# Performance work log

Hardware: AMD Instinct MI355X
Metric: run time of the kernel (lower is better)

The kernel has to match this reference:

```python
import jax, jax.numpy as jnp
import numpy as np

B, T, E, F, K = 4, 1024, 768, 24576, 32


def setup_inputs() -> dict:
    key = jax.random.key(0)
    k1, k2, k3 = jax.random.split(key, 3)
    x = jax.random.normal(k1, (B, T, E), dtype=jnp.float32)
    # kaiming_uniform-ish init for W_dec; W_enc initialized as W_dec.T (as in the module)
    bound = float(np.sqrt(6.0 / F))
    W_dec = jax.random.uniform(k2, (F, E), dtype=jnp.float32, minval=-bound, maxval=bound)
    W_enc = W_dec.T
    b_enc = jnp.zeros((F,), dtype=jnp.float32)
    b_dec = jnp.zeros((E,), dtype=jnp.float32)
    return {"x": x, "W_enc": W_enc, "W_dec": W_dec, "b_enc": b_enc, "b_dec": b_dec, "k": K}


def reference(x, W_enc, W_dec, b_enc, b_dec, k):
    # encode: (B,T,E) @ (E,F) -> (B,T,F)
    latent = jnp.einsum("bte,ef->btf", x - b_dec, W_enc) + b_enc
    # top-k mask: keep values >= k-th largest along feature dim
    kth = jax.lax.top_k(latent, k)[0][..., -1:]  # (B,T,1)
    feature_magnitudes = latent * (latent >= kth).astype(latent.dtype)
    # decode: (B,T,F) @ (F,E) -> (B,T,E)
    x_reconstructed = jnp.einsum("btf,fe->bte", feature_magnitudes, W_dec) + b_dec
    return x_reconstructed, feature_magnitudes
```

## Files before the change

kernel.cpp:

```cpp
#include <hip/hip_runtime.h>
#include <stdint.h>

#define BT_TOK 4096
#define EDIM 768
#define FDIM 24576

__device__ __forceinline__ uint32_t f2u(float f) {
    uint32_t b = __float_as_uint(f);
    return (b & 0x80000000u) ? ~b : (b | 0x80000000u);
}
__device__ __forceinline__ float u2f(uint32_t u) {
    uint32_t b = (u & 0x80000000u) ? (u & 0x7FFFFFFFu) : ~u;
    return __uint_as_float(b);
}

#define GBM 128
#define GBN 128
#define NSEG (FDIM / GBN)
#define SEGW 32
#define SEGCAP 15
#define SEGPRE (NSEG * SEGW)
#define ZCB (SEGPRE / GBN)
#define BANDCAP 160
#define T0 0.6f
#define DELTA2 0.035f

typedef int   i32x4 __attribute__((ext_vector_type(4)));
typedef float f32x4 __attribute__((ext_vector_type(4)));

__global__ __launch_bounds__(256)
void build_A_i8(const float* __restrict__ x, const float* __restrict__ bdec,
                unsigned char* __restrict__ Ai8, float* __restrict__ sxr)
{
    const int w = threadIdx.x >> 6, lane = threadIdx.x & 63;
    const int row = blockIdx.x * 4 + w;
    const float* src = x + (size_t)row * EDIM + lane * 12;
    const float* bd  = bdec + lane * 12;
    float d[12];
    #pragma unroll
    for (int t = 0; t < 3; ++t) {
        float4 v = *(const float4*)(src + t * 4);
        float4 b = *(const float4*)(bd + t * 4);
        d[t*4+0] = v.x - b.x; d[t*4+1] = v.y - b.y;
        d[t*4+2] = v.z - b.z; d[t*4+3] = v.w - b.w;
    }
    float m = 0.f;
    #pragma unroll
    for (int j = 0; j < 12; ++j) m = fmaxf(m, fabsf(d[j]));
    #pragma unroll
    for (int s = 1; s < 64; s <<= 1) m = fmaxf(m, __shfl_xor(m, s, 64));
    const float inv = (m > 0.f) ? 127.f / m : 0.f;
    if (lane == 0) sxr[row] = m / 127.f;
    uint32_t* po = (uint32_t*)(Ai8 + (size_t)row * EDIM) + lane * 3;
    #pragma unroll
    for (int t = 0; t < 3; ++t) {
        uint32_t pk = 0;
        #pragma unroll
        for (int j = 0; j < 4; ++j) {
            int q = (int)rintf(d[t*4+j] * inv);
            q = (q > 127) ? 127 : ((q < -127) ? -127 : q);
            pk |= ((uint32_t)(q & 255)) << (8 * j);
        }
        po[t] = pk;
    }
}

#define TT 64
__global__ __launch_bounds__(256)
void build_WT(const float* __restrict__ Wenc, float* __restrict__ WTf)
{
    __shared__ float tile[TT][TT + 4];
    const int n0 = blockIdx.x * TT, k0 = blockIdx.y * TT;
    const int t = threadIdx.x;

    const int krow = t >> 2, cseg = (t & 3) * 16;
    const float* src = Wenc + (size_t)(k0 + krow) * FDIM + n0 + cseg;
    float4 a0 = *(const float4*)(src);
    float4 a1 = *(const float4*)(src + 4);
    float4 a2 = *(const float4*)(src + 8);
    float4 a3 = *(const float4*)(src + 12);
    *(float4*)&tile[krow][cseg]      = a0;
    *(float4*)&tile[krow][cseg + 4]  = a1;
    *(float4*)&tile[krow][cseg + 8]  = a2;
    *(float4*)&tile[krow][cseg + 12] = a3;
    __syncthreads();

    const int nrow = t >> 2, kseg = (t & 3) * 16;
    float vals[16];
    #pragma unroll
    for (int i = 0; i < 16; ++i) vals[i] = tile[kseg + i][nrow];
    const size_t orow = (size_t)(n0 + nrow) * EDIM + k0 + kseg;
    #pragma unroll
    for (int i = 0; i < 16; i += 4)
        *(float4*)(WTf + orow + i) = make_float4(vals[i], vals[i+1], vals[i+2], vals[i+3]);
}

__global__ __launch_bounds__(256)
void quantW_i8(const float* __restrict__ WTf, unsigned char* __restrict__ Wi8,
               float* __restrict__ sw)
{
    const int w = threadIdx.x >> 6, lane = threadIdx.x & 63;
    const int row = blockIdx.x * 4 + w;
    const float* src = WTf + (size_t)row * EDIM + lane * 12;
    float d[12];
    #pragma unroll
    for (int t = 0; t < 3; ++t) {
        float4 v = *(const float4*)(src + t * 4);
        d[t*4+0] = v.x; d[t*4+1] = v.y; d[t*4+2] = v.z; d[t*4+3] = v.w;
    }
    float m = 0.f;
    #pragma unroll
    for (int j = 0; j < 12; ++j) m = fmaxf(m, fabsf(d[j]));
    #pragma unroll
    for (int s = 1; s < 64; s <<= 1) m = fmaxf(m, __shfl_xor(m, s, 64));
    const float inv = (m > 0.f) ? 127.f / m : 0.f;
    if (lane == 0) sw[row] = m / 127.f;
    uint32_t* po = (uint32_t*)(Wi8 + (size_t)row * EDIM) + lane * 3;
    #pragma unroll
    for (int t = 0; t < 3; ++t) {
        uint32_t pk = 0;
        #pragma unroll
        for (int j = 0; j < 4; ++j) {
            int q = (int)rintf(d[t*4+j] * inv);
            q = (q > 127) ? 127 : ((q < -127) ? -127 : q);
            pk |= ((uint32_t)(q & 255)) << (8 * j);
        }
        po[t] = pk;
    }
}

__device__ __forceinline__ void gld16(const unsigned char* g, void* l) {
    __builtin_amdgcn_global_load_lds(
        (const __attribute__((address_space(1))) void*)g,
        (__attribute__((address_space(3))) void*)l, 16, 0, 0);
}

__global__ __launch_bounds__(256)
void encode_i8_cand(const unsigned char* __restrict__ A,
                    const unsigned char* __restrict__ BT,
                    const float* __restrict__ benc,
                    const float* __restrict__ sxr,
                    const float* __restrict__ sw,
                    float* __restrict__ fm)
{
    __shared__ int As_i[3 * 2048];
    __shared__ int Bs_i[3 * 2048];
    __shared__ int rowcnt[GBM];

    const int tid = threadIdx.x;
    const int l = tid & 63, w = tid >> 6;
    const int wrow = (w >> 1) * 64, wcol = (w & 1) * 64;
    const int lr = l & 15, lg = l >> 4;
    const int bm = blockIdx.y * GBM, bn = blockIdx.x * GBN;
    const int cb = blockIdx.x;

    const int r0 = tid & 127, g0 = tid >> 7;
    const unsigned char* gA0 = A  + (size_t)(bm + r0) * EDIM + g0 * 16;
    const unsigned char* gA1 = A  + (size_t)(bm + r0) * EDIM + (g0 + 2) * 16;
    const unsigned char* gB0 = BT + (size_t)(bn + r0) * EDIM + g0 * 16;
    const unsigned char* gB1 = BT + (size_t)(bn + r0) * EDIM + (g0 + 2) * 16;
    int* lA0 = As_i + tid * 4;
    int* lA1 = As_i + (tid + 256) * 4;
    int* lB0 = Bs_i + tid * 4;
    int* lB1 = Bs_i + (tid + 256) * 4;

    i32x4 acc[4][4];
    #pragma unroll
    for (int i = 0; i < 4; ++i)
        #pragma unroll
        for (int j = 0; j < 4; ++j)
            acc[i][j] = (i32x4){0, 0, 0, 0};

    for (int st = 0; st < 4; ++st) {
        __syncthreads();
        #pragma unroll
        for (int t = 0; t < 3; ++t) {
            const int kt = st * 3 + t;
            gld16(gA0 + kt * 64, lA0 + t * 2048);
            gld16(gA1 + kt * 64, lA1 + t * 2048);
            gld16(gB0 + kt * 64, lB0 + t * 2048);
            gld16(gB1 + kt * 64, lB1 + t * 2048);
        }
        __syncthreads();

        #pragma unroll
        for (int t = 0; t < 3; ++t) {
            i32x4 af[4], bfr[4];
            #pragma unroll
            for (int f = 0; f < 4; ++f) {
                af[f]  = *(const i32x4*)&As_i[t * 2048 + (lg * 128 + wrow + f * 16 + lr) * 4];
                bfr[f] = *(const i32x4*)&Bs_i[t * 2048 + (lg * 128 + wcol + f * 16 + lr) * 4];
            }
            #pragma unroll
            for (int fi = 0; fi < 4; ++fi)
                #pragma unroll
                for (int fj = 0; fj < 4; ++fj)
                    acc[fi][fj] = __builtin_amdgcn_mfma_i32_16x16x64_i8(
                        af[fi], bfr[fj], acc[fi][fj], 0, 0, 0);
        }
    }

    for (int i = tid; i < GBM; i += 256) rowcnt[i] = 0;
    __syncthreads();

    float bev[4], swv[4];
    #pragma unroll
    for (int fj = 0; fj < 4; ++fj) {
        const int c = bn + wcol + fj * 16 + lr;
        bev[fj] = benc[c];
        swv[fj] = sw[c];
    }

    #pragma unroll
    for (int fi = 0; fi < 4; ++fi) {
        #pragma unroll
        for (int q = 0; q < 4; ++q) {
            const int rl = wrow + fi * 16 + lg * 4 + q;
            const float srow = sxr[bm + rl];
            uint32_t* seg = (uint32_t*)(fm + (size_t)(bm + rl) * FDIM) + (size_t)cb * SEGW;
            #pragma unroll
            for (int fj = 0; fj < 4; ++fj) {
                const float v = (float)acc[fi][fj][q] * (srow * swv[fj]) + bev[fj];
                if (v > T0) {
                    const int c = bn + wcol + fj * 16 + lr;
                    int p = atomicAdd(&rowcnt[rl], 1);
                    if (p < SEGCAP) {
                        seg[1 + p] = f2u(v);
                        seg[1 + SEGCAP + p] = (uint32_t)c;
                    }
                }
            }
        }
    }
    __syncthreads();
    for (int i = tid; i < GBM; i += 256) {
        uint32_t* seg = (uint32_t*)(fm + (size_t)(bm + i) * FDIM) + (size_t)cb * SEGW;
        seg[0] = (uint32_t)rowcnt[i];
    }

    if (cb >= ZCB) {
        const float4 z4 = make_float4(0.f, 0.f, 0.f, 0.f);
        const int rz = tid >> 5, cz = (tid & 31) * 4;
        #pragma unroll
        for (int p = 0; p < 16; ++p)
            *(float4*)(fm + (size_t)(bm + p * 8 + rz) * FDIM + bn + cz) = z4;
    }
}

__device__ __forceinline__ void sort512(uint32_t* ckey, uint32_t* cidx, int tid) {
    for (int ksz = 2; ksz <= 512; ksz <<= 1) {
        for (int j = ksz >> 1; j > 0; j >>= 1) {
            for (int i = tid; i < 512; i += 256) {
                const int ixj = i ^ j;
                if (ixj > i) {
                    uint32_t ka = ckey[i], kb = ckey[ixj];
                    uint32_t ia = cidx[i], ib = cidx[ixj];
                    bool after = (ka < kb) || (ka == kb && ia > ib);
                    bool descBlock = ((i & ksz) == 0);
                    if (descBlock ? after : !after) {
                        ckey[i] = kb; ckey[ixj] = ka;
                        cidx[i] = ib; cidx[ixj] = ia;
                    }
                }
            }
            __syncthreads();
        }
    }
}

__global__ __launch_bounds__(256)
void topk2(float* __restrict__ fm, float* __restrict__ xrec,
           const float* __restrict__ x, const float* __restrict__ WTf,
           const float* __restrict__ Wenc, const float* __restrict__ Wdec,
           const float* __restrict__ benc, const float* __restrict__ bdec,
           const int* __restrict__ kptr)
{
    const int row = blockIdx.x;
    const int tid = threadIdx.x;
    float* lrow = fm + (size_t)row * FDIM;
    const uint32_t* lrowu = (const uint32_t*)lrow;
    const float* xr = x + (size_t)row * EDIM;
    int kk = *kptr;
    if (kk < 1) kk = 1;
    if (kk > 511) kk = 511;

    __shared__ uint32_t ckey[512];
    __shared__ uint32_t cidx[512];
    __shared__ int      segc[NSEG];
    __shared__ int      scan[256];
    __shared__ double   exd[BANDCAP];
    __shared__ int      ssel[BANDCAP];
    __shared__ int      slist[BANDCAP];
    __shared__ int      redi[256];
    __shared__ float    xd[EDIM];
    __shared__ int      badf, cc;

    if (tid == 0) badf = 0;
    __syncthreads();
    for (int s = tid; s < NSEG; s += 256) {
        const int c = (int)lrowu[(size_t)s * SEGW];
        segc[s] = c;
        if (c > SEGCAP || c < 0) atomicOr(&badf, 1);
    }
    __syncthreads();

    scan[tid] = (tid < NSEG) ? segc[tid] : 0;
    __syncthreads();
    for (int d = 1; d < 256; d <<= 1) {
        int v = (tid >= d) ? scan[tid - d] : 0;
        __syncthreads();
        scan[tid] += v;
        __syncthreads();
    }
    const int total = scan[NSEG - 1];

    bool fb = (badf != 0) || (total < kk) || (total > 512) || (kk > BANDCAP);
    float t32 = 0.f;

    if (!fb) {
        for (int t = tid; t < NSEG * SEGCAP; t += 256) {
            const int s = t / SEGCAP, sl = t - s * SEGCAP;
            if (sl < segc[s]) {
                const int pos = scan[s] - segc[s] + sl;
                ckey[pos] = lrowu[(size_t)s * SEGW + 1 + sl];
                cidx[pos] = lrowu[(size_t)s * SEGW + 1 + SEGCAP + sl];
            }
        }
        for (int i = total + tid; i < 512; i += 256) { ckey[i] = 0u; cidx[i] = 0u; }
        __syncthreads();
        const float4 z4 = make_float4(0.f, 0.f, 0.f, 0.f);
        for (int i = tid * 4; i < SEGPRE; i += 1024) *(float4*)(lrow + i) = z4;
        sort512(ckey, cidx, tid);
        t32 = u2f(ckey[kk - 1]);
        if (!(t32 - DELTA2 > T0)) fb = true;
    }

    int nb = 0;
    if (!fb) {
        const float blo = t32 - DELTA2;
        int lm = 0;
        for (int j = tid; j < total; j += 256) lm += (u2f(ckey[j]) >= blo) ? 1 : 0;
        redi[tid] = lm;
        __syncthreads();
        for (int s = 128; s > 0; s >>= 1) { if (tid < s) redi[tid] += redi[tid + s]; __syncthreads(); }
        nb = redi[0];
        if (nb > BANDCAP) fb = true;
        __syncthreads();
    }

    const int e0 = tid, e1 = tid + 256, e2 = tid + 512;

    if (fb) {
        for (int e = tid; e < EDIM; e += 256) xd[e] = xr[e] - bdec[e];
        __syncthreads();
        for (int f0 = 0; f0 < FDIM; f0 += 256) {
            const int f = f0 + tid;
            float a0 = 0.f, a1 = 0.f, a2 = 0.f, a3 = 0.f;
            const float* wp = Wenc + f;
            #pragma unroll 4
            for (int e = 0; e < EDIM; e += 4) {
                a0 = fmaf(xd[e + 0], wp[(size_t)(e + 0) * FDIM], a0);
                a1 = fmaf(xd[e + 1], wp[(size_t)(e + 1) * FDIM], a1);
                a2 = fmaf(xd[e + 2], wp[(size_t)(e + 2) * FDIM], a2);
                a3 = fmaf(xd[e + 3], wp[(size_t)(e + 3) * FDIM], a3);
            }
            lrow[f] = (a0 + a1) + (a2 + a3) + benc[f];
        }
        __syncthreads();

        uint32_t ulo = 0u, uhi = 0xFFFFFFFFu, ut = f2u(T0);
        int state = 0; uint32_t kthu = 0u; int cfound = 0;
        for (int it = 0; it < 72; ++it) {
            if (uhi - ulo <= 1u) { state = 2; kthu = uhi; break; }
            if (ut <= ulo) ut = ulo + 1u;
            if (ut >= uhi) ut = uhi - 1u;
            const float t = u2f(ut);
            __syncthreads();
            if (tid == 0) cc = 0;
            __syncthreads();
            for (int i = tid * 4; i < FDIM; i += 1024) {
                float4 v = *(const float4*)(lrow + i);
                float vv[4] = {v.x, v.y, v.z, v.w};
                #pragma unroll
                for (int j = 0; j < 4; ++j) {
                    if (vv[j] > t) {
                        int p = atomicAdd(&cc, 1);
                        if (p < 512) { ckey[p] = f2u(vv[j]); cidx[p] = (uint32_t)(i + j); }
                    }
                }
            }
            __syncthreads();
            const int c = cc;
            if (c >= kk && c <= 512) { state = 1; cfound = c; break; }
            if (c < kk) uhi = ut; else ulo = ut;
            ut = ulo + ((uhi - ulo) >> 1);
        }
        if (state == 0) { state = 2; kthu = uhi; }

        if (state == 1) {
            for (int i = cfound + tid; i < 512; i += 256) { ckey[i] = 0u; cidx[i] = 0u; }
            __syncthreads();
            sort512(ckey, cidx, tid);
            const float kthf = u2f(ckey[kk - 1]);
            int lm = 0;
            for (int j = tid; j < cfound; j += 256) lm += (u2f(ckey[j]) >= kthf) ? 1 : 0;
            redi[tid] = lm;
            __syncthreads();
            for (int s = 128; s > 0; s >>= 1) { if (tid < s) redi[tid] += redi[tid + s]; __syncthreads(); }
            const int m = redi[0];

            const float4 z4 = make_float4(0.f, 0.f, 0.f, 0.f);
            for (int i = tid * 4; i < FDIM; i += 1024) *(float4*)(lrow + i) = z4;
            __syncthreads();
            for (int j = tid; j < m; j += 256) lrow[cidx[j]] = u2f(ckey[j]);

            float a0 = 0.f, a1 = 0.f, a2 = 0.f;
            for (int j = 0; j < m; ++j) {
                const float v = u2f(ckey[j]);
                const float* wr = Wdec + (size_t)cidx[j] * EDIM;
                a0 = fmaf(v, wr[e0], a0);
                a1 = fmaf(v, wr[e1], a1);
                a2 = fmaf(v, wr[e2], a2);
            }
            xrec[(size_t)row * EDIM + e0] = a0 + bdec[e0];
            xrec[(size_t)row * EDIM + e1] = a1 + bdec[e1];
            xrec[(size_t)row * EDIM + e2] = a2 + bdec[e2];
        } else {
            const float kthf = u2f(kthu);
            float a0 = 0.f, a1 = 0.f, a2 = 0.f;
            for (int basei = 0; basei < FDIM; basei += 512) {
                __syncthreads();
                if (tid == 0) cc = 0;
                __syncthreads();
                const int i = basei + tid * 2;
                float2 v = *(const float2*)(lrow + i);
                float2 o;
                o.x = (v.x >= kthf) ? v.x : 0.f;
                o.y = (v.y >= kthf) ? v.y : 0.f;
                *(float2*)(lrow + i) = o;
                if (v.x >= kthf) { int p = atomicAdd(&cc, 1); ckey[p] = __float_as_uint(v.x); cidx[p] = (uint32_t)i; }
                if (v.y >= kthf) { int p = atomicAdd(&cc, 1); ckey[p] = __float_as_uint(v.y); cidx[p] = (uint32_t)(i + 1); }
                __syncthreads();
                const int c = cc;
                for (int j = 0; j < c; ++j) {
                    const float v2 = __uint_as_float(ckey[j]);
                    const float* wr = Wdec + (size_t)cidx[j] * EDIM;
                    a0 = fmaf(v2, wr[e0], a0);
                    a1 = fmaf(v2, wr[e1], a1);
                    a2 = fmaf(v2, wr[e2], a2);
                }
            }
            xrec[(size_t)row * EDIM + e0] = a0 + bdec[e0];
            xrec[(size_t)row * EDIM + e1] = a1 + bdec[e1];
            xrec[(size_t)row * EDIM + e2] = a2 + bdec[e2];
        }
        return;
    }

    const int wv = tid >> 6, ln = tid & 63;
    for (int j = wv; j < nb; j += 4) {
        const float* wt = WTf + (size_t)cidx[j] * EDIM;
        double a0d = 0.0, a1d = 0.0, a2d = 0.0;
        {
            const int ea = ln, eb = ln + 256, ec = ln + 512;
            #pragma unroll
            for (int i = 0; i < 4; ++i) {
                a0d += ((double)xr[ea + i * 64] - (double)bdec[ea + i * 64]) * (double)wt[ea + i * 64];
                a1d += ((double)xr[eb + i * 64] - (double)bdec[eb + i * 64]) * (double)wt[eb + i * 64];
                a2d += ((double)xr[ec + i * 64] - (double)bdec[ec + i * 64]) * (double)wt[ec + i * 64];
            }
        }
        double a = a0d + a1d + a2d;
        #pragma unroll
        for (int s = 32; s > 0; s >>= 1) a += __shfl_down(a, s, 64);
        if (ln == 0) exd[j] = a + (double)benc[cidx[j]];
    }
    __syncthreads();

    for (int j = tid; j < nb; j += 256) {
        const double vj = exd[j];
        const uint32_t ij = cidx[j];
        int rank = 0;
        for (int i = 0; i < nb; ++i) {
            const double vi = exd[i];
            rank += (vi > vj || (vi == vj && (cidx[i] < ij || (cidx[i] == ij && i < j)))) ? 1 : 0;
        }
        ssel[j] = (rank < kk) ? 1 : 0;
    }
    __syncthreads();

    for (int j = tid; j < nb; j += 256) {
        if (ssel[j]) {
            const uint32_t ij = cidx[j];
            int pos = 0;
            for (int i = 0; i < nb; ++i)
                pos += (ssel[i] && (cidx[i] < ij || (cidx[i] == ij && i < j))) ? 1 : 0;
            slist[pos] = j;
        }
    }
    __syncthreads();

    for (int j = tid; j < kk; j += 256) {
        const int q = slist[j];
        lrow[cidx[q]] = (float)exd[q];
    }

    float a0 = 0.f, a1 = 0.f, a2 = 0.f;
    for (int j = 0; j < kk; ++j) {
        const int q = slist[j];
        const float v = (float)exd[q];
        const float* wr = Wdec + (size_t)cidx[q] * EDIM;
        a0 = fmaf(v, wr[e0], a0);
        a1 = fmaf(v, wr[e1], a1);
        a2 = fmaf(v, wr[e2], a2);
    }
    xrec[(size_t)row * EDIM + e0] = a0 + bdec[e0];
    xrec[(size_t)row * EDIM + e1] = a1 + bdec[e1];
    xrec[(size_t)row * EDIM + e2] = a2 + bdec[e2];
}

#define BM 128
#define BN 128
#define BKK 8
#define CAP 512

__global__ __launch_bounds__(256)
void encode_gemm(const float* __restrict__ x, const float* __restrict__ Wenc,
                 const float* __restrict__ benc, const float* __restrict__ bdec,
                 float* __restrict__ lat)
{
    __shared__ float Asf[BKK][BM];
    __shared__ float Bsf[BKK][BN];

    const int tid = threadIdx.x;
    const int tx = tid & 15, ty = tid >> 4;
    const int bm = blockIdx.y * BM;
    const int bn = blockIdx.x * BN;

    const int arow = tid >> 1, ac4 = (tid & 1) * 4;
    const int bkr  = tid >> 5, bc4 = (tid & 31) * 4;

    float acc[8][8] = {};
    float af[8], bf[8];

    for (int k0 = 0; k0 < EDIM; k0 += BKK) {
        float4 av = *(const float4*)(x + (size_t)(bm + arow) * EDIM + k0 + ac4);
        float4 bd = *(const float4*)(bdec + k0 + ac4);
        av.x -= bd.x; av.y -= bd.y; av.z -= bd.z; av.w -= bd.w;
        float4 bv = *(const float4*)(Wenc + (size_t)(k0 + bkr) * FDIM + bn + bc4);
        __syncthreads();
        Asf[ac4 + 0][arow] = av.x; Asf[ac4 + 1][arow] = av.y;
        Asf[ac4 + 2][arow] = av.z; Asf[ac4 + 3][arow] = av.w;
        *(float4*)&Bsf[bkr][bc4] = bv;
        __syncthreads();
        #pragma unroll
        for (int kkk = 0; kkk < BKK; ++kkk) {
            *(float4*)&af[0] = *(const float4*)&Asf[kkk][ty * 8];
            *(float4*)&af[4] = *(const float4*)&Asf[kkk][ty * 8 + 4];
            *(float4*)&bf[0] = *(const float4*)&Bsf[kkk][tx * 8];
            *(float4*)&bf[4] = *(const float4*)&Bsf[kkk][tx * 8 + 4];
            #pragma unroll
            for (int i = 0; i < 8; ++i)
                #pragma unroll
                for (int j = 0; j < 8; ++j)
                    acc[i][j] = fmaf(af[i], bf[j], acc[i][j]);
        }
    }

    float4 be0 = *(const float4*)(benc + bn + tx * 8);
    float4 be1 = *(const float4*)(benc + bn + tx * 8 + 4);
    #pragma unroll
    for (int i = 0; i < 8; ++i) {
        size_t ro = (size_t)(bm + ty * 8 + i) * FDIM + bn + tx * 8;
        float4 o0 = make_float4(acc[i][0] + be0.x, acc[i][1] + be0.y,
                                acc[i][2] + be0.z, acc[i][3] + be0.w);
        float4 o1 = make_float4(acc[i][4] + be1.x, acc[i][5] + be1.y,
                                acc[i][6] + be1.z, acc[i][7] + be1.w);
        *(float4*)(lat + ro)     = o0;
        *(float4*)(lat + ro + 4) = o1;
    }
}

__global__ __launch_bounds__(256)
void topk_mask_decode(float* __restrict__ lat, const float* __restrict__ Wdec,
                      const float* __restrict__ bdec, const int* __restrict__ kptr,
                      float* __restrict__ xrec)
{
    const int row = blockIdx.x;
    const int tid = threadIdx.x;
    float* lrow = lat + (size_t)row * FDIM;
    int kk = *kptr;
    if (kk < 1) kk = 1;
    if (kk > CAP) kk = CAP;

    __shared__ uint32_t ckey[CAP];
    __shared__ uint32_t cidx[CAP];
    __shared__ float redf[256];
    __shared__ int   redi[256];
    __shared__ int   cc;

    float ss = 0.f;
    for (int i = tid * 4; i < FDIM; i += 1024) {
        float4 v = *(const float4*)(lrow + i);
        ss = fmaf(v.x, v.x, fmaf(v.y, v.y, fmaf(v.z, v.z, fmaf(v.w, v.w, ss))));
    }
    redf[tid] = ss;
    __syncthreads();
    for (int s = 128; s > 0; s >>= 1) { if (tid < s) redf[tid] += redf[tid + s]; __syncthreads(); }
    const float sigma = sqrtf(redf[0] / (float)FDIM);

    uint32_t ulo = 0u, uhi = 0xFFFFFFFFu;
    uint32_t ut = f2u(2.7f * sigma);
    int state = 0; uint32_t kthu = 0u; int cfound = 0;

    for (int it = 0; it < 72; ++it) {
        if (uhi - ulo <= 1u) { state = 2; kthu = uhi; break; }
        if (ut <= ulo) ut = ulo + 1u;
        if (ut >= uhi) ut = uhi - 1u;
        const float t = u2f(ut);
        __syncthreads();
        if (tid == 0) cc = 0;
        __syncthreads();
        for (int i = tid * 4; i < FDIM; i += 1024) {
            float4 v = *(const float4*)(lrow + i);
            float vv[4] = {v.x, v.y, v.z, v.w};
            #pragma unroll
            for (int j = 0; j < 4; ++j) {
                if (vv[j] > t) {
                    int p = atomicAdd(&cc, 1);
                    if (p < CAP) { ckey[p] = f2u(vv[j]); cidx[p] = (uint32_t)(i + j); }
                }
            }
        }
        __syncthreads();
        const int c = cc;
        if (c >= kk && c <= CAP) { state = 1; cfound = c; break; }
        if (c < kk) uhi = ut; else ulo = ut;
        ut = ulo + ((uhi - ulo) >> 1);
    }
    if (state == 0) { state = 2; kthu = uhi; }

    const int e0 = tid, e1 = tid + 256, e2 = tid + 512;

    if (state == 1) {
        for (int i = cfound + tid; i < CAP; i += 256) { ckey[i] = 0u; cidx[i] = 0u; }
        __syncthreads();
        for (int ksz = 2; ksz <= CAP; ksz <<= 1) {
            for (int j = ksz >> 1; j > 0; j >>= 1) {
                for (int i = tid; i < CAP; i += 256) {
                    const int ixj = i ^ j;
                    if (ixj > i) {
                        uint32_t ka = ckey[i], kb = ckey[ixj];
                        uint32_t ia = cidx[i], ib = cidx[ixj];
                        bool after = (ka < kb) || (ka == kb && ia > ib);
                        bool descBlock = ((i & ksz) == 0);
                        if (descBlock ? after : !after) {
                            ckey[i] = kb; ckey[ixj] = ka;
                            cidx[i] = ib; cidx[ixj] = ia;
                        }
                    }
                }
                __syncthreads();
            }
        }
        const float kthf = u2f(ckey[kk - 1]);

        int lm = 0;
        for (int j2 = tid; j2 < cfound; j2 += 256) lm += (u2f(ckey[j2]) >= kthf) ? 1 : 0;
        redi[tid] = lm;
        __syncthreads();
        for (int s = 128; s > 0; s >>= 1) { if (tid < s) redi[tid] += redi[tid + s]; __syncthreads(); }
        const int m = redi[0];

        const float4 z4 = make_float4(0.f, 0.f, 0.f, 0.f);
        for (int i = tid * 4; i < FDIM; i += 1024) *(float4*)(lrow + i) = z4;
        __syncthreads();
        for (int j2 = tid; j2 < m; j2 += 256) lrow[cidx[j2]] = u2f(ckey[j2]);

        float a0 = 0.f, a1 = 0.f, a2 = 0.f;
        for (int j2 = 0; j2 < m; ++j2) {
            const float v = u2f(ckey[j2]);
            const float* wr = Wdec + (size_t)cidx[j2] * EDIM;
            a0 = fmaf(v, wr[e0], a0);
            a1 = fmaf(v, wr[e1], a1);
            a2 = fmaf(v, wr[e2], a2);
        }
        xrec[(size_t)row * EDIM + e0] = a0 + bdec[e0];
        xrec[(size_t)row * EDIM + e1] = a1 + bdec[e1];
        xrec[(size_t)row * EDIM + e2] = a2 + bdec[e2];
    } else {
        const float kthf = u2f(kthu);
        float a0 = 0.f, a1 = 0.f, a2 = 0.f;
        for (int base = 0; base < FDIM; base += 512) {
            __syncthreads();
            if (tid == 0) cc = 0;
            __syncthreads();
            const int i = base + tid * 2;
            float2 v = *(const float2*)(lrow + i);
            float2 o;
            o.x = (v.x >= kthf) ? v.x : 0.f;
            o.y = (v.y >= kthf) ? v.y : 0.f;
            *(float2*)(lrow + i) = o;
            if (v.x >= kthf) { int p = atomicAdd(&cc, 1); ckey[p] = __float_as_uint(v.x); cidx[p] = (uint32_t)i; }
            if (v.y >= kthf) { int p = atomicAdd(&cc, 1); ckey[p] = __float_as_uint(v.y); cidx[p] = (uint32_t)(i + 1); }
            __syncthreads();
            const int c = cc;
            for (int j2 = 0; j2 < c; ++j2) {
                const float v2 = __uint_as_float(ckey[j2]);
                const float* wr = Wdec + (size_t)cidx[j2] * EDIM;
                a0 = fmaf(v2, wr[e0], a0);
                a1 = fmaf(v2, wr[e1], a1);
                a2 = fmaf(v2, wr[e2], a2);
            }
        }
        xrec[(size_t)row * EDIM + e0] = a0 + bdec[e0];
        xrec[(size_t)row * EDIM + e1] = a1 + bdec[e1];
        xrec[(size_t)row * EDIM + e2] = a2 + bdec[e2];
    }
}

extern "C" void kernel_launch(void* const* d_in, const int* in_sizes, int n_in,
                              void* d_out, int out_size, void* d_ws, size_t ws_size,
                              hipStream_t stream) {
    const float* x    = (const float*)d_in[0];
    const float* Wenc = (const float*)d_in[1];
    const float* Wdec = (const float*)d_in[2];
    const float* benc = (const float*)d_in[3];
    const float* bdec = (const float*)d_in[4];
    const int*   kptr = (const int*)d_in[5];

    float* xrec = (float*)d_out;
    float* fm   = (float*)d_out + (size_t)BT_TOK * EDIM;

    const size_t szAi = (size_t)BT_TOK * EDIM;
    const size_t szWi = (size_t)FDIM * EDIM;
    const size_t szWT = (size_t)FDIM * EDIM * 4;
    const size_t szSx = (size_t)BT_TOK * 4;
    const size_t szSw = (size_t)FDIM * 4;

    if (ws_size >= szAi + szWi + szWT + szSx + szSw) {
        unsigned char* Ai8 = (unsigned char*)d_ws;
        unsigned char* Wi8 = (unsigned char*)d_ws + szAi;
        float*         WTf = (float*)((char*)d_ws + szAi + szWi);
        float*         sxr = (float*)((char*)d_ws + szAi + szWi + szWT);
        float*         sw  = (float*)((char*)d_ws + szAi + szWi + szWT + szSx);

        build_A_i8<<<BT_TOK / 4, 256, 0, stream>>>(x, bdec, Ai8, sxr);
        build_WT<<<dim3(FDIM / TT, EDIM / TT), 256, 0, stream>>>(Wenc, WTf);
        quantW_i8<<<FDIM / 4, 256, 0, stream>>>(WTf, Wi8, sw);
        encode_i8_cand<<<dim3(FDIM / GBN, BT_TOK / GBM), 256, 0, stream>>>(
            Ai8, Wi8, benc, sxr, sw, fm);
        topk2<<<BT_TOK, 256, 0, stream>>>(fm, xrec, x, WTf, Wenc, Wdec, benc, bdec, kptr);
    } else {
        dim3 g1(FDIM / BN, BT_TOK / BM);
        encode_gemm<<<g1, 256, 0, stream>>>(x, Wenc, benc, bdec, fm);
        topk_mask_decode<<<BT_TOK, 256, 0, stream>>>(fm, Wdec, bdec, kptr, xrec);
    }
}
```

Before: 514.1 us.

## Stage encode candidates in shared memory and write to separate workspace buffer

The encode kernel now collects per-row candidate segments in LDS and writes them as one coalesced int4 block to a dedicated workspace buffer, instead of scattering writes into the feature-magnitude output rows. Each block also zeroes a contiguous 64KB slab of the output up front, so the top-k kernel no longer has to re-zero the prefix region it read candidates from. This removes scattered global stores and a read-then-clear dependency on the output. The cost is an extra workspace allocation, with the old path kept as a fallback when the workspace is too small.

```diff
diff --git a/kernel.cpp b/kernel.cpp
--- a/kernel.cpp
+++ b/kernel.cpp
@@ -135,13 +135,15 @@
         (__attribute__((address_space(3))) void*)l, 16, 0, 0);
 }
 
+template<int MODE>
 __global__ __launch_bounds__(256)
 void encode_i8_cand(const unsigned char* __restrict__ A,
                     const unsigned char* __restrict__ BT,
                     const float* __restrict__ benc,
                     const float* __restrict__ sxr,
                     const float* __restrict__ sw,
-                    float* __restrict__ fm)
+                    float* __restrict__ fm,
+                    uint32_t* __restrict__ cand)
 {
     __shared__ int As_i[3 * 2048];
     __shared__ int Bs_i[3 * 2048];
@@ -153,6 +155,14 @@
     const int lr = l & 15, lg = l >> 4;
     const int bm = blockIdx.y * GBM, bn = blockIdx.x * GBN;
     const int cb = blockIdx.x;
+
+    if (MODE == 1) {
+        const int lid = blockIdx.y * gridDim.x + blockIdx.x;
+        float4* slab = (float4*)(fm + (size_t)lid * 16384);
+        const float4 z4 = make_float4(0.f, 0.f, 0.f, 0.f);
+        #pragma unroll
+        for (int i = 0; i < 16; ++i) slab[tid + i * 256] = z4;
+    }
 
     const int r0 = tid & 127, g0 = tid >> 7;
     const unsigned char* gA0 = A  + (size_t)(bm + r0) * EDIM + g0 * 16;
@@ -200,9 +210,6 @@
         }
     }
 
-    for (int i = tid; i < GBM; i += 256) rowcnt[i] = 0;
-    __syncthreads();
-
     float bev[4], swv[4];
     #pragma unroll
     for (int fj = 0; fj < 4; ++fj) {
@@ -211,39 +218,76 @@
         swv[fj] = sw[c];
     }
 
-    #pragma unroll
-    for (int fi = 0; fi < 4; ++fi) {
-        #pragma unroll
-        for (int q = 0; q < 4; ++q) {
-            const int rl = wrow + fi * 16 + lg * 4 + q;
-            const float srow = sxr[bm + rl];
-            uint32_t* seg = (uint32_t*)(fm + (size_t)(bm + rl) * FDIM) + (size_t)cb * SEGW;
+    if (MODE == 1) {
+        uint32_t* lseg = (uint32_t*)As_i;
+        __syncthreads();
+        for (int i = tid; i < 4096; i += 256) lseg[i] = 0u;
+        if (tid < GBM) rowcnt[tid] = 0;
+        __syncthreads();
+
+        #pragma unroll
+        for (int fi = 0; fi < 4; ++fi) {
             #pragma unroll
-            for (int fj = 0; fj < 4; ++fj) {
-                const float v = (float)acc[fi][fj][q] * (srow * swv[fj]) + bev[fj];
-                if (v > T0) {
-                    const int c = bn + wcol + fj * 16 + lr;
-                    int p = atomicAdd(&rowcnt[rl], 1);
-                    if (p < SEGCAP) {
-                        seg[1 + p] = f2u(v);
-                        seg[1 + SEGCAP + p] = (uint32_t)c;
+            for (int q = 0; q < 4; ++q) {
+                const int rl = wrow + fi * 16 + lg * 4 + q;
+                const float srow = sxr[bm + rl];
+                #pragma unroll
+                for (int fj = 0; fj < 4; ++fj) {
+                    const float v = (float)acc[fi][fj][q] * (srow * swv[fj]) + bev[fj];
+                    if (v > T0) {
+                        const int c = bn + wcol + fj * 16 + lr;
+                        int p = atomicAdd(&rowcnt[rl], 1);
+                        if (p < SEGCAP) {
+                            lseg[rl * SEGW + 1 + p] = f2u(v);
+                            lseg[rl * SEGW + 1 + SEGCAP + p] = (uint32_t)c;
+                        }
                     }
                 }
             }
         }
-    }
-    __syncthreads();
-    for (int i = tid; i < GBM; i += 256) {
-        uint32_t* seg = (uint32_t*)(fm + (size_t)(bm + i) * FDIM) + (size_t)cb * SEGW;
-        seg[0] = (uint32_t)rowcnt[i];
-    }
-
-    if (cb >= ZCB) {
-        const float4 z4 = make_float4(0.f, 0.f, 0.f, 0.f);
-        const int rz = tid >> 5, cz = (tid & 31) * 4;
-        #pragma unroll
-        for (int p = 0; p < 16; ++p)
-            *(float4*)(fm + (size_t)(bm + p * 8 + rz) * FDIM + bn + cz) = z4;
+        __syncthreads();
+        if (tid < GBM) lseg[tid * SEGW] = (uint32_t)rowcnt[tid];
+        __syncthreads();
+        int4* dst = (int4*)(cand + ((size_t)cb * BT_TOK + bm) * SEGW);
+        const int4* srcl = (const int4*)lseg;
+        #pragma unroll
+        for (int i = 0; i < 4; ++i) dst[tid + i * 256] = srcl[tid + i * 256];
+    } else {
+        for (int i = tid; i < GBM; i += 256) rowcnt[i] = 0;
+        __syncthreads();
+        #pragma unroll
+        for (int fi = 0; fi < 4; ++fi) {
+            #pragma unroll
+            for (int q = 0; q < 4; ++q) {
+                const int rl = wrow + fi * 16 + lg * 4 + q;
+                const float srow = sxr[bm + rl];
+                uint32_t* seg = (uint32_t*)(fm + (size_t)(bm + rl) * FDIM) + (size_t)cb * SEGW;
+                #pragma unroll
+                for (int fj = 0; fj < 4; ++fj) {
+                    const float v = (float)acc[fi][fj][q] * (srow * swv[fj]) + bev[fj];
+                    if (v > T0) {
+                        const int c = bn + wcol + fj * 16 + lr;
+                        int p = atomicAdd(&rowcnt[rl], 1);
+                        if (p < SEGCAP) {
+                            seg[1 + p] = f2u(v);
+                            seg[1 + SEGCAP + p] = (uint32_t)c;
+                        }
+                    }
+                }
+            }
+        }
+        __syncthreads();
+        for (int i = tid; i < GBM; i += 256) {
+            uint32_t* seg = (uint32_t*)(fm + (size_t)(bm + i) * FDIM) + (size_t)cb * SEGW;
+            seg[0] = (uint32_t)rowcnt[i];
+        }
+        if (cb >= ZCB) {
+            const float4 z4 = make_float4(0.f, 0.f, 0.f, 0.f);
+            const int rz = tid >> 5, cz = (tid & 31) * 4;
+            #pragma unroll
+            for (int p = 0; p < 16; ++p)
+                *(float4*)(fm + (size_t)(bm + p * 8 + rz) * FDIM + bn + cz) = z4;
+        }
     }
 }
 
@@ -268,12 +312,13 @@
     }
 }
 
+template<int MODE>
 __global__ __launch_bounds__(256)
 void topk2(float* __restrict__ fm, float* __restrict__ xrec,
            const float* __restrict__ x, const float* __restrict__ WTf,
            const float* __restrict__ Wenc, const float* __restrict__ Wdec,
            const float* __restrict__ benc, const float* __restrict__ bdec,
-           const int* __restrict__ kptr)
+           const int* __restrict__ kptr, const uint32_t* __restrict__ cand)
 {
     const int row = blockIdx.x;
     const int tid = threadIdx.x;
@@ -298,7 +343,9 @@
     if (tid == 0) badf = 0;
     __syncthreads();
     for (int s = tid; s < NSEG; s += 256) {
-        const int c = (int)lrowu[(size_t)s * SEGW];
+        const int c = (MODE == 0)
+            ? (int)lrowu[(size_t)s * SEGW]
+            : (int)cand[((size_t)s * BT_TOK + row) * SEGW];
         segc[s] = c;
         if (c > SEGCAP || c < 0) atomicOr(&badf, 1);
     }
@@ -322,14 +369,22 @@
             const int s = t / SEGCAP, sl = t - s * SEGCAP;
             if (sl < segc[s]) {
                 const int pos = scan[s] - segc[s] + sl;
-                ckey[pos] = lrowu[(size_t)s * SEGW + 1 + sl];
-                cidx[pos] = lrowu[(size_t)s * SEGW + 1 + SEGCAP + sl];
+                if (MODE == 0) {
+                    ckey[pos] = lrowu[(size_t)s * SEGW + 1 + sl];
+                    cidx[pos] = lrowu[(size_t)s * SEGW + 1 + SEGCAP + sl];
+                } else {
+                    const size_t b = ((size_t)s * BT_TOK + row) * SEGW;
+                    ckey[pos] = cand[b + 1 + sl];
+                    cidx[pos] = cand[b + 1 + SEGCAP + sl];
+                }
             }
         }
         for (int i = total + tid; i < 512; i += 256) { ckey[i] = 0u; cidx[i] = 0u; }
         __syncthreads();
-        const float4 z4 = make_float4(0.f, 0.f, 0.f, 0.f);
-        for (int i = tid * 4; i < SEGPRE; i += 1024) *(float4*)(lrow + i) = z4;
+        if (MODE == 0) {
+            const float4 z4 = make_float4(0.f, 0.f, 0.f, 0.f);
+            for (int i = tid * 4; i < SEGPRE; i += 1024) *(float4*)(lrow + i) = z4;
+        }
         sort512(ckey, cidx, tid);
         t32 = u2f(ckey[kk - 1]);
         if (!(t32 - DELTA2 > T0)) fb = true;
@@ -737,20 +792,31 @@
     const size_t szWT = (size_t)FDIM * EDIM * 4;
     const size_t szSx = (size_t)BT_TOK * 4;
     const size_t szSw = (size_t)FDIM * 4;
-
-    if (ws_size >= szAi + szWi + szWT + szSx + szSw) {
+    const size_t base = szAi + szWi + szWT + szSx + szSw;
+    const size_t szCd = (size_t)NSEG * BT_TOK * SEGW * 4;
+
+    if (ws_size >= base) {
         unsigned char* Ai8 = (unsigned char*)d_ws;
         unsigned char* Wi8 = (unsigned char*)d_ws + szAi;
         float*         WTf = (float*)((char*)d_ws + szAi + szWi);
         float*         sxr = (float*)((char*)d_ws + szAi + szWi + szWT);
         float*         sw  = (float*)((char*)d_ws + szAi + szWi + szWT + szSx);
+        uint32_t*      cnd = (uint32_t*)((char*)d_ws + base);
 
         build_A_i8<<<BT_TOK / 4, 256, 0, stream>>>(x, bdec, Ai8, sxr);
         build_WT<<<dim3(FDIM / TT, EDIM / TT), 256, 0, stream>>>(Wenc, WTf);
         quantW_i8<<<FDIM / 4, 256, 0, stream>>>(WTf, Wi8, sw);
-        encode_i8_cand<<<dim3(FDIM / GBN, BT_TOK / GBM), 256, 0, stream>>>(
-            Ai8, Wi8, benc, sxr, sw, fm);
-        topk2<<<BT_TOK, 256, 0, stream>>>(fm, xrec, x, WTf, Wenc, Wdec, benc, bdec, kptr);
+        if (ws_size >= base + szCd) {
+            encode_i8_cand<1><<<dim3(FDIM / GBN, BT_TOK / GBM), 256, 0, stream>>>(
+                Ai8, Wi8, benc, sxr, sw, fm, cnd);
+            topk2<1><<<BT_TOK, 256, 0, stream>>>(fm, xrec, x, WTf, Wenc, Wdec,
+                                                 benc, bdec, kptr, cnd);
+        } else {
+            encode_i8_cand<0><<<dim3(FDIM / GBN, BT_TOK / GBM), 256, 0, stream>>>(
+                Ai8, Wi8, benc, sxr, sw, fm, nullptr);
+            topk2<0><<<BT_TOK, 256, 0, stream>>>(fm, xrec, x, WTf, Wenc, Wdec,
+                                                 benc, bdec, kptr, nullptr);
+        }
     } else {
         dim3 g1(FDIM / BN, BT_TOK / BM);
         encode_gemm<<<g1, 256, 0, stream>>>(x, Wenc, benc, bdec, fm);
```

Measured after the change: 509.0 us. No clear change (-1.0%).
